# Optimization experiments

Hardware: AMD Instinct MI355X
Metric: run time of the kernel (lower is better)

## Reference

```python
import jax, jax.numpy as jnp
import numpy as np

B, S, E = 8, 2048, 512
VOCAB, FVOCAB = 32000, 128
SCALE = float(np.power(E, 0.5))  # emb_size ** (0.5 * temper), temper=1


def setup_inputs() -> dict:
    key = jax.random.key(0)
    ks = jax.random.split(key, 7)
    key_seq = jax.random.randint(ks[0], (B, S), 0, VOCAB, dtype=jnp.int32)
    value_seq = jax.random.randint(ks[1], (B, S), 0, FVOCAB, dtype=jnp.int32)
    hidden = jax.random.normal(ks[2], (B, S, E), dtype=jnp.float32)
    mask_matrix = jax.random.uniform(ks[3], (B, S, S), dtype=jnp.float32)
    nan_matrix = jnp.zeros((1,), dtype=jnp.int32)  # unused by forward
    # learned params; padding_idx=0 -> zero row in embeddings
    key_emb = jax.random.normal(ks[4], (VOCAB, E), dtype=jnp.float32).at[0].set(0.0)
    value_emb = jax.random.normal(ks[5], (FVOCAB, E), dtype=jnp.float32).at[0].set(0.0)
    weight = jax.random.normal(ks[6], (E, E), dtype=jnp.float32) / np.sqrt(E)
    return {
        "key_seq": key_seq, "value_seq": value_seq, "hidden": hidden,
        "mask_matrix": mask_matrix, "nan_matrix": nan_matrix,
        "key_emb": key_emb, "value_emb": value_emb, "weight": weight,
    }


def reference(key_seq, value_seq, hidden, mask_matrix, nan_matrix,
              key_emb, value_emb, weight):
    k = key_emb[key_seq]          # [B,S,E]
    v = value_emb[value_seq]      # [B,S,E]
    q = jnp.einsum('bsd,de->bse', hidden, weight)   # hidden @ weight
    u = jnp.einsum('bse,bte->bst', q, k) / SCALE    # QK^T, [B,S,S]
    mask = jnp.clip(mask_matrix.astype(u.dtype), 0.0, 1.0)
    exp_u = jnp.exp(u)
    delta = exp_u * mask
    p = delta / (jnp.sum(delta, axis=2, keepdims=True) + 1e-10)
    o = jnp.einsum('bst,bte->bse', p, v)            # PV, [B,S,E]
    return o
```

## Files before the change

kernel.cpp:

```cpp
#include <hip/hip_runtime.h>
#include <stdint.h>

#define BB 8
#define SS 2048
#define EE 512
#define INV_SCALE 0.04419417382415922f

typedef __attribute__((ext_vector_type(8))) short bf8_t;
typedef __attribute__((ext_vector_type(4))) float f4_t;

__device__ __forceinline__ unsigned short f2bf(float f) {
    union { float f; uint32_t u; } x; x.f = f;
    uint32_t r = x.u + 0x7fffu + ((x.u >> 16) & 1u);
    return (unsigned short)(r >> 16);
}


__global__ void __launch_bounds__(256) gather_k_kernel(const int* __restrict__ idx,
                                                       const float* __restrict__ emb,
                                                       unsigned short* __restrict__ out) {
    int id = blockIdx.x * 256 + threadIdx.x;
    int chunk = id & 63;
    int row = id >> 6;
    int e0 = chunk * 8;
    int k = idx[row];
    const float* src = emb + (size_t)k * EE + e0;
    float4 a = *(const float4*)(src);
    float4 c = *(const float4*)(src + 4);
    union { unsigned short s[8]; int4 v; } u;
    u.s[0] = f2bf(a.x); u.s[1] = f2bf(a.y); u.s[2] = f2bf(a.z); u.s[3] = f2bf(a.w);
    u.s[4] = f2bf(c.x); u.s[5] = f2bf(c.y); u.s[6] = f2bf(c.z); u.s[7] = f2bf(c.w);
    *(int4*)(out + (size_t)row * EE + e0) = u.v;
}

__global__ void __launch_bounds__(256) cast_h_kernel(const float* __restrict__ in,
                                                     unsigned short* __restrict__ out) {
    int id = blockIdx.x * 256 + threadIdx.x;
    const float* src = in + (size_t)id * 8;
    float4 a = *(const float4*)(src);
    float4 c = *(const float4*)(src + 4);
    union { unsigned short s[8]; int4 v; } u;
    u.s[0] = f2bf(a.x); u.s[1] = f2bf(a.y); u.s[2] = f2bf(a.z); u.s[3] = f2bf(a.w);
    u.s[4] = f2bf(c.x); u.s[5] = f2bf(c.y); u.s[6] = f2bf(c.z); u.s[7] = f2bf(c.w);
    *(int4*)(out + (size_t)id * 8) = u.v;
}

__global__ void __launch_bounds__(256) gather_vt_kernel(const int* __restrict__ idx,
                                                        const float* __restrict__ emb,
                                                        unsigned short* __restrict__ vt) {
    int id = blockIdx.x * 256 + threadIdx.x;
    int t8 = id & 255;
    int rest = id >> 8;
    int e = rest & (EE - 1);
    int b = rest >> 9;
    int t0 = t8 * 8;
    const int* ip = idx + b * SS + t0;
    int4 i0 = *(const int4*)(ip);
    int4 i1 = *(const int4*)(ip + 4);
    union { unsigned short s[8]; int4 v; } u;
    u.s[0] = f2bf(emb[(size_t)i0.x * EE + e]);
    u.s[1] = f2bf(emb[(size_t)i0.y * EE + e]);
    u.s[2] = f2bf(emb[(size_t)i0.z * EE + e]);
    u.s[3] = f2bf(emb[(size_t)i0.w * EE + e]);
    u.s[4] = f2bf(emb[(size_t)i1.x * EE + e]);
    u.s[5] = f2bf(emb[(size_t)i1.y * EE + e]);
    u.s[6] = f2bf(emb[(size_t)i1.z * EE + e]);
    u.s[7] = f2bf(emb[(size_t)i1.w * EE + e]);
    *(int4*)(vt + ((size_t)b * EE + e) * SS + t0) = u.v;
}

__global__ void __launch_bounds__(256) transpose_w_kernel(const float* __restrict__ w,
                                                          unsigned short* __restrict__ wt) {
    int id = blockIdx.x * 256 + threadIdx.x;
    int e = id & (EE - 1);
    int f = id >> 9;
    wt[id] = f2bf(w[(size_t)e * EE + f] * INV_SCALE);
}


__device__ __forceinline__ void stage128(const unsigned short* gbase, int ld,
                                         unsigned short* lds, int wave, int lane) {
#pragma unroll
    for (int p = 0; p < 2; ++p) {
        int row = p * 64 + lane;
        const unsigned short* g = gbase + (size_t)row * ld + wave * 8;
        unsigned short* l = lds + wave * 1024 + p * 512 + lane * 8;
        __builtin_amdgcn_global_load_lds((const __attribute__((address_space(1))) unsigned int*)g,
                                         (__attribute__((address_space(3))) unsigned int*)l,
                                         16, 0, 0);
    }
}

__device__ __forceinline__ void frag_mfma(const unsigned short* As, const unsigned short* Bs,
                                          f4_t acc[4][4], int wm, int wn, int quad, int l16) {
    bf8_t af[4], bfr[4];
#pragma unroll
    for (int mi = 0; mi < 4; ++mi)
        af[mi] = *(const bf8_t*)(As + quad * 1024 + (wm * 64 + mi * 16 + l16) * 8);
#pragma unroll
    for (int ni = 0; ni < 4; ++ni)
        bfr[ni] = *(const bf8_t*)(Bs + quad * 1024 + (wn * 64 + ni * 16 + l16) * 8);
#pragma unroll
    for (int mi = 0; mi < 4; ++mi)
#pragma unroll
        for (int ni = 0; ni < 4; ++ni)
            acc[mi][ni] = __builtin_amdgcn_mfma_f32_16x16x32_bf16(af[mi], bfr[ni],
                                                                  acc[mi][ni], 0, 0, 0);
}

template <int KLEN>
__device__ __forceinline__ void mfma_loop_128(const unsigned short* Abase, int lda,
                                              const unsigned short* Bbase, int ldb,
                                              unsigned short* As, unsigned short* Bs,
                                              f4_t acc[4][4], int wave, int lane) {
    const int wm = wave >> 1, wn = wave & 1;
    const int quad = lane >> 4, l16 = lane & 15;
#pragma unroll 1
    for (int k0 = 0; k0 < KLEN; k0 += 32) {
        stage128(Abase + k0, lda, As, wave, lane);
        stage128(Bbase + k0, ldb, Bs, wave, lane);
        __syncthreads();
        frag_mfma(As, Bs, acc, wm, wn, quad, l16);
        __syncthreads();
    }
}


__global__ void __launch_bounds__(256) qgen_kernel(const unsigned short* __restrict__ H,
                                                   const unsigned short* __restrict__ Wt,
                                                   unsigned short* __restrict__ Q) {
    __shared__ unsigned short As[128 * 32];
    __shared__ unsigned short Bs[128 * 32];
    const int tid = threadIdx.x, wave = tid >> 6, lane = tid & 63;
    const int rowT = blockIdx.y;
    const int colT = blockIdx.x;
    f4_t acc[4][4];
    const f4_t z = {0.f, 0.f, 0.f, 0.f};
    for (int i = 0; i < 4; ++i) for (int j = 0; j < 4; ++j) acc[i][j] = z;
    mfma_loop_128<EE>(H + (size_t)rowT * 128 * EE, EE,
                      Wt + (size_t)colT * 128 * EE, EE, As, Bs, acc, wave, lane);
    const int wm = wave >> 1, wn = wave & 1, quad = lane >> 4, l16 = lane & 15;
#pragma unroll
    for (int mi = 0; mi < 4; ++mi)
#pragma unroll
        for (int r = 0; r < 4; ++r) {
            int row = rowT * 128 + wm * 64 + mi * 16 + quad * 4 + r;
#pragma unroll
            for (int ni = 0; ni < 4; ++ni) {
                int col = colT * 128 + wn * 64 + ni * 16 + l16;
                Q[(size_t)row * EE + col] = f2bf(acc[mi][ni][r]);
            }
        }
}

__global__ void __launch_bounds__(256) qk_kernel(const unsigned short* __restrict__ Q,
                                                 const unsigned short* __restrict__ K,
                                                 const float* __restrict__ mask,
                                                 unsigned short* __restrict__ delta,
                                                 float* __restrict__ lsum) {
    __shared__ unsigned short As[128 * 32];
    __shared__ unsigned short Bs[128 * 32];
    __shared__ float Ms[128 * 128];
    const int tid = threadIdx.x, wave = tid >> 6, lane = tid & 63;
    const int b = blockIdx.z, qT = blockIdx.y, tT = blockIdx.x;
    const int wm = wave >> 1, wn = wave & 1, quad = lane >> 4, l16 = lane & 15;

    const unsigned short* Abase = Q + ((size_t)b * SS + qT * 128) * EE;
    const unsigned short* Bbase = K + ((size_t)b * SS + tT * 128) * EE;
    const float* mbase = mask + ((size_t)b * SS + qT * 128) * SS + tT * 128;

    f4_t acc[4][4];
    const f4_t z = {0.f, 0.f, 0.f, 0.f};
    for (int i = 0; i < 4; ++i) for (int j = 0; j < 4; ++j) acc[i][j] = z;

#pragma unroll 1
    for (int it = 0; it < 16; ++it) {
        {
            int g = it * 256 + tid;
            const float* msrc = mbase + (size_t)(g >> 5) * SS + (g & 31) * 4;
            float* mdst = Ms + (size_t)g * 4;
            __builtin_amdgcn_global_load_lds((const __attribute__((address_space(1))) unsigned int*)msrc,
                                             (__attribute__((address_space(3))) unsigned int*)mdst,
                                             16, 0, 0);
        }
        stage128(Abase + it * 32, EE, As, wave, lane);
        stage128(Bbase + it * 32, EE, Bs, wave, lane);
        __syncthreads();
        frag_mfma(As, Bs, acc, wm, wn, quad, l16);
        __syncthreads();
    }

#pragma unroll
    for (int mi = 0; mi < 4; ++mi)
#pragma unroll
        for (int r = 0; r < 4; ++r) {
            int rloc = wm * 64 + mi * 16 + quad * 4 + r;
            int row = qT * 128 + rloc;
            unsigned short* drow = delta + ((size_t)b * SS + row) * SS;
            float psum = 0.f;
#pragma unroll
            for (int ni = 0; ni < 4; ++ni) {
                int cloc = wn * 64 + ni * 16 + l16;
                float m = Ms[rloc * 128 + cloc];
                m = fminf(fmaxf(m, 0.f), 1.f);
                float e = __expf(acc[mi][ni][r]) * m;
                drow[tT * 128 + cloc] = f2bf(e);
                psum += e;
            }
#pragma unroll
            for (int off = 1; off < 16; off <<= 1)
                psum += __shfl_xor(psum, off, 16);
            if (l16 == 0) atomicAdd(&lsum[b * SS + row], psum);
        }
}

__global__ void __launch_bounds__(256) pv_kernel(const unsigned short* __restrict__ delta,
                                                 const unsigned short* __restrict__ Vt,
                                                 const float* __restrict__ lsum,
                                                 float* __restrict__ out) {
    __shared__ unsigned short As[128 * 32];
    __shared__ unsigned short Bs[128 * 32];
    const int tid = threadIdx.x, wave = tid >> 6, lane = tid & 63;
    const int b = blockIdx.z, qT = blockIdx.y, eT = blockIdx.x;
    const int wm = wave >> 1, wn = wave & 1, quad = lane >> 4, l16 = lane & 15;

    float inv[4][4];
#pragma unroll
    for (int mi = 0; mi < 4; ++mi)
#pragma unroll
        for (int r = 0; r < 4; ++r) {
            int row = qT * 128 + wm * 64 + mi * 16 + quad * 4 + r;
            inv[mi][r] = lsum[b * SS + row];
        }
#pragma unroll
    for (int mi = 0; mi < 4; ++mi)
#pragma unroll
        for (int r = 0; r < 4; ++r)
            inv[mi][r] = 1.0f / (inv[mi][r] + 1e-10f);

    f4_t acc[4][4];
    const f4_t z = {0.f, 0.f, 0.f, 0.f};
    for (int i = 0; i < 4; ++i) for (int j = 0; j < 4; ++j) acc[i][j] = z;
    mfma_loop_128<SS>(delta + ((size_t)b * SS + qT * 128) * SS, SS,
                      Vt + ((size_t)b * EE + eT * 128) * SS, SS, As, Bs, acc, wave, lane);

#pragma unroll
    for (int mi = 0; mi < 4; ++mi)
#pragma unroll
        for (int r = 0; r < 4; ++r) {
            int row = qT * 128 + wm * 64 + mi * 16 + quad * 4 + r;
#pragma unroll
            for (int ni = 0; ni < 4; ++ni) {
                int col = eT * 128 + wn * 64 + ni * 16 + l16;
                out[((size_t)b * SS + row) * EE + col] = acc[mi][ni][r] * inv[mi][r];
            }
        }
}


extern "C" void kernel_launch(void* const* d_in, const int* in_sizes, int n_in,
                              void* d_out, int out_size, void* d_ws, size_t ws_size,
                              hipStream_t stream) {
    const int*   key_seq = (const int*)d_in[0];
    const int*   val_seq = (const int*)d_in[1];
    const float* hidden  = (const float*)d_in[2];
    const float* mask    = (const float*)d_in[3];
    const float* key_emb = (const float*)d_in[5];
    const float* val_emb = (const float*)d_in[6];
    const float* weight  = (const float*)d_in[7];
    float* out = (float*)d_out;

    char* ws = (char*)d_ws;
    const size_t SZ_BSE = (size_t)BB * SS * EE * sizeof(unsigned short);
    unsigned short* Q    = (unsigned short*)(ws);
    unsigned short* K    = (unsigned short*)(ws + SZ_BSE);
    unsigned short* Vt   = (unsigned short*)(ws + 2 * SZ_BSE);
    unsigned short* H    = (unsigned short*)(ws + 3 * SZ_BSE);
    unsigned short* Wt   = (unsigned short*)(ws + 4 * SZ_BSE);
    float*          lsum = (float*)(ws + 4 * SZ_BSE + 524288);
    unsigned short* delta= (unsigned short*)(ws + 4 * SZ_BSE + 524288 + 65536);

    hipMemsetAsync(lsum, 0, (size_t)BB * SS * sizeof(float), stream);

    gather_k_kernel<<<4096, 256, 0, stream>>>(key_seq, key_emb, K);
    cast_h_kernel<<<4096, 256, 0, stream>>>(hidden, H);
    gather_vt_kernel<<<4096, 256, 0, stream>>>(val_seq, val_emb, Vt);
    transpose_w_kernel<<<1024, 256, 0, stream>>>(weight, Wt);

    qgen_kernel<<<dim3(4, 128), 256, 0, stream>>>(H, Wt, Q);
    qk_kernel<<<dim3(16, 16, 8), 256, 0, stream>>>(Q, K, mask, delta, lsum);
    pv_kernel<<<dim3(4, 16, 8), 256, 0, stream>>>(delta, Vt, lsum, out);
}
```

Baseline: 494.0 us.

## Switch GEMM kernels to single-wave 64x64 tiles with 4-stage async LDS pipeline

Each of the three GEMM kernels now runs one wave per block on a 64x64 tile. The wave stages K-slices into a 4-deep LDS ring with global_load_lds and uses s_waitcnt vmcnt counters in place of __syncthreads. The goal is to remove block-wide barriers and overlap global loads with MFMA work. The qk kernel also reads the mask straight from global memory in the epilogue instead of staging it in LDS. The trade-off is less tile reuse, since operand traffic per output roughly doubles with 64x64 tiles, and four times as many blocks.

```diff
diff --git a/kernel.cpp b/kernel.cpp
--- a/kernel.cpp
+++ b/kernel.cpp
@@ -78,133 +78,134 @@
 }
 
 
-__device__ __forceinline__ void stage128(const unsigned short* gbase, int ld,
-                                         unsigned short* lds, int wave, int lane) {
-#pragma unroll
-    for (int p = 0; p < 2; ++p) {
-        int row = p * 64 + lane;
-        const unsigned short* g = gbase + (size_t)row * ld + wave * 8;
-        unsigned short* l = lds + wave * 1024 + p * 512 + lane * 8;
+#define WAITV16() asm volatile("s_waitcnt vmcnt(16)" ::: "memory")
+#define WAITV8()  asm volatile("s_waitcnt vmcnt(8)"  ::: "memory")
+#define WAITV0()  asm volatile("s_waitcnt vmcnt(0)"  ::: "memory")
+#define MEMORDER() asm volatile("" ::: "memory")
+
+__device__ __forceinline__ void stageAB(const unsigned short* Ab, int lda,
+                                        const unsigned short* Bb, int ldb, int k0,
+                                        unsigned short* dA, unsigned short* dB, int lane) {
+#pragma unroll
+    for (int p = 0; p < 4; ++p) {
+        const unsigned short* g = Ab + (size_t)lane * lda + k0 + p * 8;
         __builtin_amdgcn_global_load_lds((const __attribute__((address_space(1))) unsigned int*)g,
-                                         (__attribute__((address_space(3))) unsigned int*)l,
-                                         16, 0, 0);
+            (__attribute__((address_space(3))) unsigned int*)(dA + p * 512 + lane * 8), 16, 0, 0);
     }
-}
-
-__device__ __forceinline__ void frag_mfma(const unsigned short* As, const unsigned short* Bs,
-                                          f4_t acc[4][4], int wm, int wn, int quad, int l16) {
-    bf8_t af[4], bfr[4];
-#pragma unroll
-    for (int mi = 0; mi < 4; ++mi)
-        af[mi] = *(const bf8_t*)(As + quad * 1024 + (wm * 64 + mi * 16 + l16) * 8);
+#pragma unroll
+    for (int p = 0; p < 4; ++p) {
+        const unsigned short* g = Bb + (size_t)lane * ldb + k0 + p * 8;
+        __builtin_amdgcn_global_load_lds((const __attribute__((address_space(1))) unsigned int*)g,
+            (__attribute__((address_space(3))) unsigned int*)(dB + p * 512 + lane * 8), 16, 0, 0);
+    }
+}
+
+__device__ __forceinline__ void read_frags(const unsigned short* sA, const unsigned short* sB,
+                                           bf8_t af[4], bf8_t bf[4], int quad, int l16) {
+#pragma unroll
+    for (int mi = 0; mi < 4; ++mi)
+        af[mi] = *(const bf8_t*)(sA + quad * 512 + (mi * 16 + l16) * 8);
 #pragma unroll
     for (int ni = 0; ni < 4; ++ni)
-        bfr[ni] = *(const bf8_t*)(Bs + quad * 1024 + (wn * 64 + ni * 16 + l16) * 8);
+        bf[ni] = *(const bf8_t*)(sB + quad * 512 + (ni * 16 + l16) * 8);
+}
+
+__device__ __forceinline__ void do_mfma(const bf8_t af[4], const bf8_t bf[4], f4_t acc[4][4]) {
 #pragma unroll
     for (int mi = 0; mi < 4; ++mi)
 #pragma unroll
         for (int ni = 0; ni < 4; ++ni)
-            acc[mi][ni] = __builtin_amdgcn_mfma_f32_16x16x32_bf16(af[mi], bfr[ni],
+            acc[mi][ni] = __builtin_amdgcn_mfma_f32_16x16x32_bf16(af[mi], bf[ni],
                                                                   acc[mi][ni], 0, 0, 0);
 }
 
-template <int KLEN>
-__device__ __forceinline__ void mfma_loop_128(const unsigned short* Abase, int lda,
-                                              const unsigned short* Bbase, int ldb,
-                                              unsigned short* As, unsigned short* Bs,
-                                              f4_t acc[4][4], int wave, int lane) {
-    const int wm = wave >> 1, wn = wave & 1;
-    const int quad = lane >> 4, l16 = lane & 15;
+template <int NIT>
+__device__ __forceinline__ void wave_gemm(const unsigned short* Ab, int lda,
+                                          const unsigned short* Bb, int ldb,
+                                          unsigned short (*sA)[2048], unsigned short (*sB)[2048],
+                                          f4_t acc[4][4], int lane, int quad, int l16) {
+    stageAB(Ab, lda, Bb, ldb, 0,  sA[0], sB[0], lane);
+    stageAB(Ab, lda, Bb, ldb, 32, sA[1], sB[1], lane);
+    stageAB(Ab, lda, Bb, ldb, 64, sA[2], sB[2], lane);
+    bf8_t af[4], bf[4];
 #pragma unroll 1
-    for (int k0 = 0; k0 < KLEN; k0 += 32) {
-        stage128(Abase + k0, lda, As, wave, lane);
-        stage128(Bbase + k0, ldb, Bs, wave, lane);
-        __syncthreads();
-        frag_mfma(As, Bs, acc, wm, wn, quad, l16);
-        __syncthreads();
+    for (int it = 0; it < NIT - 3; ++it) {
+        WAITV16();
+        int buf = it & 3;
+        read_frags(sA[buf], sB[buf], af, bf, quad, l16);
+        stageAB(Ab, lda, Bb, ldb, (it + 3) * 32, sA[(it + 3) & 3], sB[(it + 3) & 3], lane);
+        do_mfma(af, bf, acc);
     }
-}
-
-
-__global__ void __launch_bounds__(256) qgen_kernel(const unsigned short* __restrict__ H,
-                                                   const unsigned short* __restrict__ Wt,
-                                                   unsigned short* __restrict__ Q) {
-    __shared__ unsigned short As[128 * 32];
-    __shared__ unsigned short Bs[128 * 32];
-    const int tid = threadIdx.x, wave = tid >> 6, lane = tid & 63;
-    const int rowT = blockIdx.y;
-    const int colT = blockIdx.x;
+    WAITV16();
+    read_frags(sA[(NIT - 3) & 3], sB[(NIT - 3) & 3], af, bf, quad, l16);
+    do_mfma(af, bf, acc);
+    WAITV8();
+    read_frags(sA[(NIT - 2) & 3], sB[(NIT - 2) & 3], af, bf, quad, l16);
+    do_mfma(af, bf, acc);
+    WAITV0();
+    read_frags(sA[(NIT - 1) & 3], sB[(NIT - 1) & 3], af, bf, quad, l16);
+    do_mfma(af, bf, acc);
+}
+
+
+__global__ void __launch_bounds__(64) qgen_kernel(const unsigned short* __restrict__ H,
+                                                  const unsigned short* __restrict__ Wt,
+                                                  unsigned short* __restrict__ Q) {
+    __shared__ __align__(16) unsigned short sA[4][2048];
+    __shared__ __align__(16) unsigned short sB[4][2048];
+    const int lane = threadIdx.x, quad = lane >> 4, l16 = lane & 15;
+    const int mT = blockIdx.x, fT = blockIdx.y;
     f4_t acc[4][4];
     const f4_t z = {0.f, 0.f, 0.f, 0.f};
     for (int i = 0; i < 4; ++i) for (int j = 0; j < 4; ++j) acc[i][j] = z;
-    mfma_loop_128<EE>(H + (size_t)rowT * 128 * EE, EE,
-                      Wt + (size_t)colT * 128 * EE, EE, As, Bs, acc, wave, lane);
-    const int wm = wave >> 1, wn = wave & 1, quad = lane >> 4, l16 = lane & 15;
+    wave_gemm<16>(H + (size_t)mT * 64 * EE, EE, Wt + (size_t)fT * 64 * EE, EE,
+                  sA, sB, acc, lane, quad, l16);
 #pragma unroll
     for (int mi = 0; mi < 4; ++mi)
 #pragma unroll
         for (int r = 0; r < 4; ++r) {
-            int row = rowT * 128 + wm * 64 + mi * 16 + quad * 4 + r;
+            int row = mT * 64 + mi * 16 + quad * 4 + r;
 #pragma unroll
             for (int ni = 0; ni < 4; ++ni) {
-                int col = colT * 128 + wn * 64 + ni * 16 + l16;
+                int col = fT * 64 + ni * 16 + l16;
                 Q[(size_t)row * EE + col] = f2bf(acc[mi][ni][r]);
             }
         }
 }
 
-__global__ void __launch_bounds__(256) qk_kernel(const unsigned short* __restrict__ Q,
-                                                 const unsigned short* __restrict__ K,
-                                                 const float* __restrict__ mask,
-                                                 unsigned short* __restrict__ delta,
-                                                 float* __restrict__ lsum) {
-    __shared__ unsigned short As[128 * 32];
-    __shared__ unsigned short Bs[128 * 32];
-    __shared__ float Ms[128 * 128];
-    const int tid = threadIdx.x, wave = tid >> 6, lane = tid & 63;
-    const int b = blockIdx.z, qT = blockIdx.y, tT = blockIdx.x;
-    const int wm = wave >> 1, wn = wave & 1, quad = lane >> 4, l16 = lane & 15;
-
-    const unsigned short* Abase = Q + ((size_t)b * SS + qT * 128) * EE;
-    const unsigned short* Bbase = K + ((size_t)b * SS + tT * 128) * EE;
-    const float* mbase = mask + ((size_t)b * SS + qT * 128) * SS + tT * 128;
-
+__global__ void __launch_bounds__(64) qk_kernel(const unsigned short* __restrict__ Q,
+                                                const unsigned short* __restrict__ K,
+                                                const float* __restrict__ mask,
+                                                unsigned short* __restrict__ delta,
+                                                float* __restrict__ lsum) {
+    __shared__ __align__(16) unsigned short sA[4][2048];
+    __shared__ __align__(16) unsigned short sB[4][2048];
+    const int lane = threadIdx.x, quad = lane >> 4, l16 = lane & 15;
+    const int qT = blockIdx.x, tT = blockIdx.y, b = blockIdx.z;
     f4_t acc[4][4];
     const f4_t z = {0.f, 0.f, 0.f, 0.f};
     for (int i = 0; i < 4; ++i) for (int j = 0; j < 4; ++j) acc[i][j] = z;
-
-#pragma unroll 1
-    for (int it = 0; it < 16; ++it) {
-        {
-            int g = it * 256 + tid;
-            const float* msrc = mbase + (size_t)(g >> 5) * SS + (g & 31) * 4;
-            float* mdst = Ms + (size_t)g * 4;
-            __builtin_amdgcn_global_load_lds((const __attribute__((address_space(1))) unsigned int*)msrc,
-                                             (__attribute__((address_space(3))) unsigned int*)mdst,
-                                             16, 0, 0);
-        }
-        stage128(Abase + it * 32, EE, As, wave, lane);
-        stage128(Bbase + it * 32, EE, Bs, wave, lane);
-        __syncthreads();
-        frag_mfma(As, Bs, acc, wm, wn, quad, l16);
-        __syncthreads();
-    }
-
+    wave_gemm<16>(Q + ((size_t)b * SS + qT * 64) * EE, EE,
+                  K + ((size_t)b * SS + tT * 64) * EE, EE,
+                  sA, sB, acc, lane, quad, l16);
 #pragma unroll
     for (int mi = 0; mi < 4; ++mi)
 #pragma unroll
         for (int r = 0; r < 4; ++r) {
-            int rloc = wm * 64 + mi * 16 + quad * 4 + r;
-            int row = qT * 128 + rloc;
-            unsigned short* drow = delta + ((size_t)b * SS + row) * SS;
+            int rloc = mi * 16 + quad * 4 + r;
+            int row = qT * 64 + rloc;
+            const float* mrow = mask + ((size_t)b * SS + row) * SS + tT * 64;
+            unsigned short* drow = delta + ((size_t)b * SS + row) * SS + tT * 64;
+            float mv[4];
+#pragma unroll
+            for (int ni = 0; ni < 4; ++ni)
+                mv[ni] = mrow[ni * 16 + l16];
             float psum = 0.f;
 #pragma unroll
             for (int ni = 0; ni < 4; ++ni) {
-                int cloc = wn * 64 + ni * 16 + l16;
-                float m = Ms[rloc * 128 + cloc];
-                m = fminf(fmaxf(m, 0.f), 1.f);
+                float m = fminf(fmaxf(mv[ni], 0.f), 1.f);
                 float e = __expf(acc[mi][ni][r]) * m;
-                drow[tT * 128 + cloc] = f2bf(e);
+                drow[ni * 16 + l16] = f2bf(e);
                 psum += e;
             }
 #pragma unroll
@@ -214,45 +215,37 @@
         }
 }
 
-__global__ void __launch_bounds__(256) pv_kernel(const unsigned short* __restrict__ delta,
-                                                 const unsigned short* __restrict__ Vt,
-                                                 const float* __restrict__ lsum,
-                                                 float* __restrict__ out) {
-    __shared__ unsigned short As[128 * 32];
-    __shared__ unsigned short Bs[128 * 32];
-    const int tid = threadIdx.x, wave = tid >> 6, lane = tid & 63;
-    const int b = blockIdx.z, qT = blockIdx.y, eT = blockIdx.x;
-    const int wm = wave >> 1, wn = wave & 1, quad = lane >> 4, l16 = lane & 15;
-
-    float inv[4][4];
-#pragma unroll
-    for (int mi = 0; mi < 4; ++mi)
-#pragma unroll
-        for (int r = 0; r < 4; ++r) {
-            int row = qT * 128 + wm * 64 + mi * 16 + quad * 4 + r;
-            inv[mi][r] = lsum[b * SS + row];
-        }
+__global__ void __launch_bounds__(64) pv_kernel(const unsigned short* __restrict__ delta,
+                                                const unsigned short* __restrict__ Vt,
+                                                const float* __restrict__ lsum,
+                                                float* __restrict__ out) {
+    __shared__ __align__(16) unsigned short sA[4][2048];
+    __shared__ __align__(16) unsigned short sB[4][2048];
+    const int lane = threadIdx.x, quad = lane >> 4, l16 = lane & 15;
+    const int qT = blockIdx.x, eT = blockIdx.y, b = blockIdx.z;
+    float lv[4][4];
 #pragma unroll
     for (int mi = 0; mi < 4; ++mi)
 #pragma unroll
         for (int r = 0; r < 4; ++r)
-            inv[mi][r] = 1.0f / (inv[mi][r] + 1e-10f);
-
+            lv[mi][r] = lsum[b * SS + qT * 64 + mi * 16 + quad * 4 + r];
+    MEMORDER();
     f4_t acc[4][4];
     const f4_t z = {0.f, 0.f, 0.f, 0.f};
     for (int i = 0; i < 4; ++i) for (int j = 0; j < 4; ++j) acc[i][j] = z;
-    mfma_loop_128<SS>(delta + ((size_t)b * SS + qT * 128) * SS, SS,
-                      Vt + ((size_t)b * EE + eT * 128) * SS, SS, As, Bs, acc, wave, lane);
-
+    wave_gemm<64>(delta + ((size_t)b * SS + qT * 64) * SS, SS,
+                  Vt + ((size_t)b * EE + eT * 64) * SS, SS,
+                  sA, sB, acc, lane, quad, l16);
 #pragma unroll
     for (int mi = 0; mi < 4; ++mi)
 #pragma unroll
         for (int r = 0; r < 4; ++r) {
-            int row = qT * 128 + wm * 64 + mi * 16 + quad * 4 + r;
+            int row = qT * 64 + mi * 16 + quad * 4 + r;
+            float iv = 1.0f / (lv[mi][r] + 1e-10f);
 #pragma unroll
             for (int ni = 0; ni < 4; ++ni) {
-                int col = eT * 128 + wn * 64 + ni * 16 + l16;
-                out[((size_t)b * SS + row) * EE + col] = acc[mi][ni][r] * inv[mi][r];
+                int col = eT * 64 + ni * 16 + l16;
+                out[((size_t)b * SS + row) * EE + col] = acc[mi][ni][r] * iv;
             }
         }
 }
@@ -287,7 +280,7 @@
     gather_vt_kernel<<<4096, 256, 0, stream>>>(val_seq, val_emb, Vt);
     transpose_w_kernel<<<1024, 256, 0, stream>>>(weight, Wt);
 
-    qgen_kernel<<<dim3(4, 128), 256, 0, stream>>>(H, Wt, Q);
-    qk_kernel<<<dim3(16, 16, 8), 256, 0, stream>>>(Q, K, mask, delta, lsum);
-    pv_kernel<<<dim3(4, 16, 8), 256, 0, stream>>>(delta, Vt, lsum, out);
-}
+    qgen_kernel<<<dim3(256, 8), 64, 0, stream>>>(H, Wt, Q);
+    qk_kernel<<<dim3(32, 32, 8), 64, 0, stream>>>(Q, K, mask, delta, lsum);
+    pv_kernel<<<dim3(32, 8, 8), 64, 0, stream>>>(delta, Vt, lsum, out);
+}
```

Result: slower. 639.0 us (+29.4%).

## Double the GEMM K-tile to 64, read mask directly in epilogue, reorder PV grid

Applied to the files above, without the earlier changes.

The shared MFMA loop now stages a 64-wide K slice per barrier pair instead of 32, which halves the number of __syncthreads and loop iterations in all three GEMM kernels. The QK kernel drops its 64KB LDS mask staging and reads the mask straight from global memory in the epilogue, so LDS use falls enough for the new 3-blocks-per-CU launch bound. The PV grid is reordered so q-tiles vary fastest, which changes how delta and Vt tiles are shared in cache. The cost is more LDS per K-tile, and mask loads that can no longer overlap the QK matmul loop.

```diff
diff --git a/kernel.cpp b/kernel.cpp
--- a/kernel.cpp
+++ b/kernel.cpp
@@ -78,67 +78,65 @@
 }
 
 
-__device__ __forceinline__ void stage128(const unsigned short* gbase, int ld,
-                                         unsigned short* lds, int wave, int lane) {
-#pragma unroll
-    for (int p = 0; p < 2; ++p) {
-        int row = p * 64 + lane;
-        const unsigned short* g = gbase + (size_t)row * ld + wave * 8;
-        unsigned short* l = lds + wave * 1024 + p * 512 + lane * 8;
+__device__ __forceinline__ void stage_bk64(const unsigned short* gbase, int ld, int k0,
+                                           unsigned short* lds, int wave, int lane) {
+#pragma unroll
+    for (int p = 0; p < 4; ++p) {
+        int c = p * 4 + wave;
+        int kc = c >> 1, half = c & 1;
+        const unsigned short* g = gbase + (size_t)(half * 64 + lane) * ld + k0 + kc * 8;
+        unsigned short* l = lds + kc * 1024 + half * 512 + lane * 8;
         __builtin_amdgcn_global_load_lds((const __attribute__((address_space(1))) unsigned int*)g,
                                          (__attribute__((address_space(3))) unsigned int*)l,
                                          16, 0, 0);
     }
 }
 
-__device__ __forceinline__ void frag_mfma(const unsigned short* As, const unsigned short* Bs,
-                                          f4_t acc[4][4], int wm, int wn, int quad, int l16) {
-    bf8_t af[4], bfr[4];
-#pragma unroll
-    for (int mi = 0; mi < 4; ++mi)
-        af[mi] = *(const bf8_t*)(As + quad * 1024 + (wm * 64 + mi * 16 + l16) * 8);
-#pragma unroll
-    for (int ni = 0; ni < 4; ++ni)
-        bfr[ni] = *(const bf8_t*)(Bs + quad * 1024 + (wn * 64 + ni * 16 + l16) * 8);
-#pragma unroll
-    for (int mi = 0; mi < 4; ++mi)
-#pragma unroll
-        for (int ni = 0; ni < 4; ++ni)
-            acc[mi][ni] = __builtin_amdgcn_mfma_f32_16x16x32_bf16(af[mi], bfr[ni],
-                                                                  acc[mi][ni], 0, 0, 0);
-}
-
 template <int KLEN>
-__device__ __forceinline__ void mfma_loop_128(const unsigned short* Abase, int lda,
-                                              const unsigned short* Bbase, int ldb,
-                                              unsigned short* As, unsigned short* Bs,
-                                              f4_t acc[4][4], int wave, int lane) {
+__device__ __forceinline__ void mfma_loop64(const unsigned short* Abase, int lda,
+                                            const unsigned short* Bbase, int ldb,
+                                            unsigned short* As, unsigned short* Bs,
+                                            f4_t acc[4][4], int wave, int lane) {
     const int wm = wave >> 1, wn = wave & 1;
     const int quad = lane >> 4, l16 = lane & 15;
 #pragma unroll 1
-    for (int k0 = 0; k0 < KLEN; k0 += 32) {
-        stage128(Abase + k0, lda, As, wave, lane);
-        stage128(Bbase + k0, ldb, Bs, wave, lane);
+    for (int k0 = 0; k0 < KLEN; k0 += 64) {
+        stage_bk64(Abase, lda, k0, As, wave, lane);
+        stage_bk64(Bbase, ldb, k0, Bs, wave, lane);
         __syncthreads();
-        frag_mfma(As, Bs, acc, wm, wn, quad, l16);
+#pragma unroll
+        for (int kk = 0; kk < 2; ++kk) {
+            bf8_t af[4], bfr[4];
+#pragma unroll
+            for (int mi = 0; mi < 4; ++mi)
+                af[mi] = *(const bf8_t*)(As + ((kk * 4 + quad) * 128 + wm * 64 + mi * 16 + l16) * 8);
+#pragma unroll
+            for (int ni = 0; ni < 4; ++ni)
+                bfr[ni] = *(const bf8_t*)(Bs + ((kk * 4 + quad) * 128 + wn * 64 + ni * 16 + l16) * 8);
+#pragma unroll
+            for (int mi = 0; mi < 4; ++mi)
+#pragma unroll
+                for (int ni = 0; ni < 4; ++ni)
+                    acc[mi][ni] = __builtin_amdgcn_mfma_f32_16x16x32_bf16(af[mi], bfr[ni],
+                                                                          acc[mi][ni], 0, 0, 0);
+        }
         __syncthreads();
     }
 }
 
 
-__global__ void __launch_bounds__(256) qgen_kernel(const unsigned short* __restrict__ H,
-                                                   const unsigned short* __restrict__ Wt,
-                                                   unsigned short* __restrict__ Q) {
-    __shared__ unsigned short As[128 * 32];
-    __shared__ unsigned short Bs[128 * 32];
+__global__ void __launch_bounds__(256, 3) qgen_kernel(const unsigned short* __restrict__ H,
+                                                      const unsigned short* __restrict__ Wt,
+                                                      unsigned short* __restrict__ Q) {
+    __shared__ __align__(16) unsigned short As[128 * 64];
+    __shared__ __align__(16) unsigned short Bs[128 * 64];
     const int tid = threadIdx.x, wave = tid >> 6, lane = tid & 63;
-    const int rowT = blockIdx.y;
-    const int colT = blockIdx.x;
+    const int rowT = blockIdx.y, colT = blockIdx.x;
     f4_t acc[4][4];
     const f4_t z = {0.f, 0.f, 0.f, 0.f};
     for (int i = 0; i < 4; ++i) for (int j = 0; j < 4; ++j) acc[i][j] = z;
-    mfma_loop_128<EE>(H + (size_t)rowT * 128 * EE, EE,
-                      Wt + (size_t)colT * 128 * EE, EE, As, Bs, acc, wave, lane);
+    mfma_loop64<EE>(H + (size_t)rowT * 128 * EE, EE,
+                    Wt + (size_t)colT * 128 * EE, EE, As, Bs, acc, wave, lane);
     const int wm = wave >> 1, wn = wave & 1, quad = lane >> 4, l16 = lane & 15;
 #pragma unroll
     for (int mi = 0; mi < 4; ++mi)
@@ -153,58 +151,40 @@
         }
 }
 
-__global__ void __launch_bounds__(256) qk_kernel(const unsigned short* __restrict__ Q,
-                                                 const unsigned short* __restrict__ K,
-                                                 const float* __restrict__ mask,
-                                                 unsigned short* __restrict__ delta,
-                                                 float* __restrict__ lsum) {
-    __shared__ unsigned short As[128 * 32];
-    __shared__ unsigned short Bs[128 * 32];
-    __shared__ float Ms[128 * 128];
+__global__ void __launch_bounds__(256, 3) qk_kernel(const unsigned short* __restrict__ Q,
+                                                    const unsigned short* __restrict__ K,
+                                                    const float* __restrict__ mask,
+                                                    unsigned short* __restrict__ delta,
+                                                    float* __restrict__ lsum) {
+    __shared__ __align__(16) unsigned short As[128 * 64];
+    __shared__ __align__(16) unsigned short Bs[128 * 64];
     const int tid = threadIdx.x, wave = tid >> 6, lane = tid & 63;
     const int b = blockIdx.z, qT = blockIdx.y, tT = blockIdx.x;
     const int wm = wave >> 1, wn = wave & 1, quad = lane >> 4, l16 = lane & 15;
 
-    const unsigned short* Abase = Q + ((size_t)b * SS + qT * 128) * EE;
-    const unsigned short* Bbase = K + ((size_t)b * SS + tT * 128) * EE;
-    const float* mbase = mask + ((size_t)b * SS + qT * 128) * SS + tT * 128;
-
     f4_t acc[4][4];
     const f4_t z = {0.f, 0.f, 0.f, 0.f};
     for (int i = 0; i < 4; ++i) for (int j = 0; j < 4; ++j) acc[i][j] = z;
-
-#pragma unroll 1
-    for (int it = 0; it < 16; ++it) {
-        {
-            int g = it * 256 + tid;
-            const float* msrc = mbase + (size_t)(g >> 5) * SS + (g & 31) * 4;
-            float* mdst = Ms + (size_t)g * 4;
-            __builtin_amdgcn_global_load_lds((const __attribute__((address_space(1))) unsigned int*)msrc,
-                                             (__attribute__((address_space(3))) unsigned int*)mdst,
-                                             16, 0, 0);
-        }
-        stage128(Abase + it * 32, EE, As, wave, lane);
-        stage128(Bbase + it * 32, EE, Bs, wave, lane);
-        __syncthreads();
-        frag_mfma(As, Bs, acc, wm, wn, quad, l16);
-        __syncthreads();
-    }
+    mfma_loop64<EE>(Q + ((size_t)b * SS + qT * 128) * EE, EE,
+                    K + ((size_t)b * SS + tT * 128) * EE, EE, As, Bs, acc, wave, lane);
 
 #pragma unroll
     for (int mi = 0; mi < 4; ++mi)
 #pragma unroll
         for (int r = 0; r < 4; ++r) {
-            int rloc = wm * 64 + mi * 16 + quad * 4 + r;
-            int row = qT * 128 + rloc;
-            unsigned short* drow = delta + ((size_t)b * SS + row) * SS;
+            int row = qT * 128 + wm * 64 + mi * 16 + quad * 4 + r;
+            const float* mrow = mask + ((size_t)b * SS + row) * SS + tT * 128;
+            unsigned short* drow = delta + ((size_t)b * SS + row) * SS + tT * 128;
+            float mv[4];
+#pragma unroll
+            for (int ni = 0; ni < 4; ++ni)
+                mv[ni] = mrow[wn * 64 + ni * 16 + l16];
             float psum = 0.f;
 #pragma unroll
             for (int ni = 0; ni < 4; ++ni) {
-                int cloc = wn * 64 + ni * 16 + l16;
-                float m = Ms[rloc * 128 + cloc];
-                m = fminf(fmaxf(m, 0.f), 1.f);
+                float m = fminf(fmaxf(mv[ni], 0.f), 1.f);
                 float e = __expf(acc[mi][ni][r]) * m;
-                drow[tT * 128 + cloc] = f2bf(e);
+                drow[wn * 64 + ni * 16 + l16] = f2bf(e);
                 psum += e;
             }
 #pragma unroll
@@ -214,45 +194,39 @@
         }
 }
 
-__global__ void __launch_bounds__(256) pv_kernel(const unsigned short* __restrict__ delta,
-                                                 const unsigned short* __restrict__ Vt,
-                                                 const float* __restrict__ lsum,
-                                                 float* __restrict__ out) {
-    __shared__ unsigned short As[128 * 32];
-    __shared__ unsigned short Bs[128 * 32];
+__global__ void __launch_bounds__(256, 3) pv_kernel(const unsigned short* __restrict__ delta,
+                                                    const unsigned short* __restrict__ Vt,
+                                                    const float* __restrict__ lsum,
+                                                    float* __restrict__ out) {
+    __shared__ __align__(16) unsigned short As[128 * 64];
+    __shared__ __align__(16) unsigned short Bs[128 * 64];
     const int tid = threadIdx.x, wave = tid >> 6, lane = tid & 63;
-    const int b = blockIdx.z, qT = blockIdx.y, eT = blockIdx.x;
+    const int b = blockIdx.z, eT = blockIdx.y, qT = blockIdx.x;
     const int wm = wave >> 1, wn = wave & 1, quad = lane >> 4, l16 = lane & 15;
 
-    float inv[4][4];
-#pragma unroll
-    for (int mi = 0; mi < 4; ++mi)
-#pragma unroll
-        for (int r = 0; r < 4; ++r) {
-            int row = qT * 128 + wm * 64 + mi * 16 + quad * 4 + r;
-            inv[mi][r] = lsum[b * SS + row];
-        }
+    float lv[4][4];
 #pragma unroll
     for (int mi = 0; mi < 4; ++mi)
 #pragma unroll
         for (int r = 0; r < 4; ++r)
-            inv[mi][r] = 1.0f / (inv[mi][r] + 1e-10f);
+            lv[mi][r] = lsum[b * SS + qT * 128 + wm * 64 + mi * 16 + quad * 4 + r];
 
     f4_t acc[4][4];
     const f4_t z = {0.f, 0.f, 0.f, 0.f};
     for (int i = 0; i < 4; ++i) for (int j = 0; j < 4; ++j) acc[i][j] = z;
-    mfma_loop_128<SS>(delta + ((size_t)b * SS + qT * 128) * SS, SS,
-                      Vt + ((size_t)b * EE + eT * 128) * SS, SS, As, Bs, acc, wave, lane);
+    mfma_loop64<SS>(delta + ((size_t)b * SS + qT * 128) * SS, SS,
+                    Vt + ((size_t)b * EE + eT * 128) * SS, SS, As, Bs, acc, wave, lane);
 
 #pragma unroll
     for (int mi = 0; mi < 4; ++mi)
 #pragma unroll
         for (int r = 0; r < 4; ++r) {
             int row = qT * 128 + wm * 64 + mi * 16 + quad * 4 + r;
+            float iv = 1.0f / (lv[mi][r] + 1e-10f);
 #pragma unroll
             for (int ni = 0; ni < 4; ++ni) {
                 int col = eT * 128 + wn * 64 + ni * 16 + l16;
-                out[((size_t)b * SS + row) * EE + col] = acc[mi][ni][r] * inv[mi][r];
+                out[((size_t)b * SS + row) * EE + col] = acc[mi][ni][r] * iv;
             }
         }
 }
@@ -289,5 +263,5 @@
 
     qgen_kernel<<<dim3(4, 128), 256, 0, stream>>>(H, Wt, Q);
     qk_kernel<<<dim3(16, 16, 8), 256, 0, stream>>>(Q, K, mask, delta, lsum);
-    pv_kernel<<<dim3(4, 16, 8), 256, 0, stream>>>(delta, Vt, lsum, out);
-}
+    pv_kernel<<<dim3(16, 4, 8), 256, 0, stream>>>(delta, Vt, lsum, out);
+}
```

New measurement: 493.9 us. Within noise of the previous version (-0.0%).
